# Performance work log

Measured on AMD Instinct MI355X. Metric: run time of the kernel, lower is better.

Reference implementation:

```python
import jax, jax.numpy as jnp
import numpy as np

TAU = 2.0      # LIF membrane time constant
VTH = 1.0      # spike threshold
ALPHA = 2.0    # surrogate-gradient sharpness (atan surrogate)
EPS = 1e-5     # BatchNorm eps

@jax.custom_vjp
def spike(u):
    return (u > 0.0).astype(u.dtype)

def _spike_fwd(u):
    return spike(u), u

def _spike_bwd(u, g):
    sg = ALPHA / (2.0 * (1.0 + (jnp.pi / 2.0 * ALPHA * u) ** 2))
    return (g * sg,)

spike.defvjp(_spike_fwd, _spike_bwd)

def lif_time(x):
    # x: [B,T,C,H,W] -> spikes [B,T,C,H,W]; hard-reset LIF, v0 = 0
    xT = jnp.moveaxis(x, 1, 0)  # [T,B,C,H,W]
    def step(v, xt):
        v = v + (xt - v) / TAU
        s = spike(v - VTH)
        return v * (1.0 - s), s
    _, sT = jax.lax.scan(step, jnp.zeros_like(xT[0]), xT)
    return jnp.moveaxis(sT, 0, 1)

def conv2d(x, w, stride, pad):
    return jax.lax.conv_general_dilated(
        x, w, (stride, stride), [(pad, pad), (pad, pad)],
        dimension_numbers=('NCHW', 'OIHW', 'NCHW'))

def bn(x, gamma, beta, mean, var):
    # inference-style BatchNorm2d with running stats; x: [N,C,H,W]
    inv = gamma * jax.lax.rsqrt(var + EPS)
    return x * inv[None, :, None, None] + (beta - mean * inv)[None, :, None, None]

def setup_inputs() -> dict:
    key = jax.random.key(0)
    ks = jax.random.split(key, 16)
    B, T, Cin, Cout, H, W = 16, 8, 128, 256, 56, 56
    d = {}
    d['x_spike'] = (jax.random.uniform(ks[0], (B, T, Cin, H, W)) < 0.2).astype(jnp.float32)
    d['conv1_w'] = jax.random.normal(ks[1], (Cout, Cin, 3, 3), dtype=jnp.float32) * 0.05
    d['conv2_w'] = jax.random.normal(ks[2], (Cout, Cout, 3, 3), dtype=jnp.float32) * 0.05
    d['ds_w'] = jax.random.normal(ks[3], (Cout, Cin, 1, 1), dtype=jnp.float32) * 0.05
    for i, p in enumerate(['n1', 'n2', 'nd']):
        d[p + '_gamma'] = 1.0 + 0.1 * jax.random.normal(ks[4 + i], (Cout,), dtype=jnp.float32)
        d[p + '_beta'] = 0.1 * jax.random.normal(ks[7 + i], (Cout,), dtype=jnp.float32)
        d[p + '_mean'] = 0.01 * jax.random.normal(ks[10 + i], (Cout,), dtype=jnp.float32)
        d[p + '_var'] = jax.random.uniform(ks[13 + i], (Cout,), minval=0.5, maxval=1.5)
    return d

def reference(x_spike, conv1_w, conv2_w, ds_w,
              n1_gamma, n1_beta, n1_mean, n1_var,
              n2_gamma, n2_beta, n2_mean, n2_var,
              nd_gamma, nd_beta, nd_mean, nd_var):
    B, T, Cin, H, W = x_spike.shape
    x_flat = x_spike.reshape(B * T, Cin, H, W)
    # downsample shortcut (1x1 conv stride 2 + BN)
    identity = bn(conv2d(x_flat, ds_w, 2, 0), nd_gamma, nd_beta, nd_mean, nd_var)
    # NOTE: original module runs lif_shortcut on identity but DISCARDS the result
    # (pure state side-effect); it does not affect the output, so it is omitted.
    out = bn(conv2d(x_flat, conv1_w, 2, 1), n1_gamma, n1_beta, n1_mean, n1_var)
    Cout, Ho, Wo = out.shape[1], out.shape[2], out.shape[3]
    out = lif_time(out.reshape(B, T, Cout, Ho, Wo))
    out = bn(conv2d(out.reshape(B * T, Cout, Ho, Wo), conv2_w, 1, 1),
             n2_gamma, n2_beta, n2_mean, n2_var) + identity
    return lif_time(out.reshape(B, T, Cout, Ho, Wo))
```

## Files before the change

### kernel.cpp

```cpp
#include <hip/hip_runtime.h>
#include <hip/hip_bf16.h>

#define CIN  128
#define CO   256
#define HIN  56
#define WIN  56
#define OH   28
#define OWW  28
#define P    784
#define HWIN 3136
#define PERT 200704

typedef __attribute__((ext_vector_type(8))) short bf16x8v;
typedef __attribute__((ext_vector_type(4))) float f32x4;

__device__ __forceinline__ f32x4 mfma16(bf16x8v a, bf16x8v b, f32x4 c) {
    return __builtin_amdgcn_mfma_f32_16x16x32_bf16(a, b, c, 0, 0, 0);
}

__device__ __forceinline__ void gld_lds16(const void* g, void* l) {
    __builtin_amdgcn_global_load_lds(
        (const __attribute__((address_space(1))) void*)g,
        (__attribute__((address_space(3))) void*)l, 16, 0, 0);
}

__global__ __launch_bounds__(256) void k_prep_bias(
    const float* __restrict__ g1, const float* __restrict__ b1,
    const float* __restrict__ m1, const float* __restrict__ v1,
    const float* __restrict__ g2, const float* __restrict__ b2,
    const float* __restrict__ m2, const float* __restrict__ v2,
    const float* __restrict__ gd, const float* __restrict__ bd,
    const float* __restrict__ md, const float* __restrict__ vd,
    float* __restrict__ inv1o, float* __restrict__ bias1o,
    float* __restrict__ inv2o, float* __restrict__ invdo,
    float* __restrict__ bias2o)
{
    int co = threadIdx.x;
    float inv1 = g1[co] / sqrtf(v1[co] + 1e-5f);
    float inv2 = g2[co] / sqrtf(v2[co] + 1e-5f);
    float invd = gd[co] / sqrtf(vd[co] + 1e-5f);
    inv1o[co]  = inv1;
    bias1o[co] = fmaf(-m1[co], inv1, b1[co]);
    inv2o[co]  = inv2;
    invdo[co]  = invd;
    bias2o[co] = fmaf(-m2[co], inv2, b2[co]) + fmaf(-md[co], invd, bd[co]);
}

__global__ __launch_bounds__(256) void k_prep_w2p(
    const float* __restrict__ w2, const float* __restrict__ inv2,
    unsigned short* __restrict__ hi, unsigned short* __restrict__ lo)
{
    int i = blockIdx.x * 256 + threadIdx.x;
    if (i >= 73728) return;
    int tap = i >> 13;
    int r   = i & 8191;
    int ch  = r >> 10;
    int r2  = r & 1023;
    int cf  = r2 >> 6;
    int lane = r2 & 63;
    int co  = cf * 16 + (lane & 15);
    int cib = ch * 32 + (lane >> 4) * 8;
#pragma unroll
    for (int j = 0; j < 8; j++) {
        float w = w2[((size_t)co * CO + cib + j) * 9 + tap] * inv2[co];
        __hip_bfloat16 h = __float2bfloat16(w);
        __hip_bfloat16 l = __float2bfloat16(w - __bfloat162float(h));
        hi[(size_t)i * 8 + j] = *(unsigned short*)&h;
        lo[(size_t)i * 8 + j] = *(unsigned short*)&l;
    }
}

__global__ __launch_bounds__(256) void k_prep_w1p(
    const float* __restrict__ w1, const float* __restrict__ inv1,
    unsigned short* __restrict__ hi, unsigned short* __restrict__ mid,
    unsigned short* __restrict__ lo)
{
    int i = blockIdx.x * 256 + threadIdx.x;
    if (i >= 36864) return;
    int tap = i >> 12;
    int r   = i & 4095;
    int ch  = r >> 10;
    int r2  = r & 1023;
    int cf  = r2 >> 6;
    int lane = r2 & 63;
    int co  = cf * 16 + (lane & 15);
    int cib = ch * 32 + (lane >> 4) * 8;
#pragma unroll
    for (int j = 0; j < 8; j++) {
        float w = w1[((size_t)co * CIN + cib + j) * 9 + tap] * inv1[co];
        __hip_bfloat16 h = __float2bfloat16(w);
        float r1 = w - __bfloat162float(h);
        __hip_bfloat16 m = __float2bfloat16(r1);
        float r2f = r1 - __bfloat162float(m);
        __hip_bfloat16 l = __float2bfloat16(r2f);
        hi[(size_t)i * 8 + j]  = *(unsigned short*)&h;
        mid[(size_t)i * 8 + j] = *(unsigned short*)&m;
        lo[(size_t)i * 8 + j]  = *(unsigned short*)&l;
    }
}

__global__ __launch_bounds__(256) void k_prep_wdp(
    const float* __restrict__ wd, const float* __restrict__ invd,
    unsigned short* __restrict__ hi, unsigned short* __restrict__ lo)
{
    int i = blockIdx.x * 256 + threadIdx.x;
    if (i >= 4096) return;
    int ch  = i >> 10;
    int r2  = i & 1023;
    int cf  = r2 >> 6;
    int lane = r2 & 63;
    int co  = cf * 16 + (lane & 15);
    int cib = ch * 32 + (lane >> 4) * 8;
#pragma unroll
    for (int j = 0; j < 8; j++) {
        float w = wd[(size_t)co * CIN + cib + j] * invd[co];
        __hip_bfloat16 h = __float2bfloat16(w);
        __hip_bfloat16 l = __float2bfloat16(w - __bfloat162float(h));
        hi[(size_t)i * 8 + j] = *(unsigned short*)&h;
        lo[(size_t)i * 8 + j] = *(unsigned short*)&l;
    }
}

__global__ __launch_bounds__(256) void k_pack1(
    const float* __restrict__ x, unsigned int* __restrict__ xt_p)
{
    int i = blockIdx.x * 256 + threadIdx.x;
    int pos = i % HWIN;
    int nw  = i / HWIN;
    int w   = nw & 3;
    int n   = nw >> 2;
    const float* xp = x + ((size_t)n * CIN + w * 32) * HWIN + pos;
    unsigned int word = 0;
#pragma unroll
    for (int ci = 0; ci < 32; ci++)
        if (xp[(size_t)ci * HWIN] != 0.f) word |= (1u << ci);
    xt_p[((size_t)n * HWIN + pos) * 4 + w] = word;
}

__global__ __launch_bounds__(256) void k_conv1_mfma(
    const unsigned int* __restrict__ xt_p,
    const unsigned short* __restrict__ w1hip,
    const unsigned short* __restrict__ w1midp,
    const unsigned short* __restrict__ w1lop,
    const float* __restrict__ bias1,
    float* __restrict__ out)
{
    __shared__ unsigned int XW[4 * 522];

    const int n    = blockIdx.x / 7;
    const int rt   = blockIdx.x - n * 7;
    const int r0   = rt * 4;
    const int tid  = threadIdx.x;
    const int wave = tid >> 6;
    const int lane = tid & 63;
    const int l15  = lane & 15;
    const int quad = lane >> 4;
    const int cf0  = blockIdx.y * 8 + wave * 2;

    const unsigned int* xp_n = xt_p + (size_t)n * HWIN * 4;
    for (int i = tid; i < 513; i += 256) {
        int row = i / 57, c = i - row * 57;
        int irow = 2 * r0 - 1 + row;
        int iw   = c - 1;
        uint4 val = {0u, 0u, 0u, 0u};
        if (irow >= 0 && iw >= 0)
            val = *(const uint4*)(xp_n + (size_t)(irow * WIN + iw) * 4);
        int base = row * 58 + c;
        XW[0 * 522 + base] = val.x;
        XW[1 * 522 + base] = val.y;
        XW[2 * 522 + base] = val.z;
        XW[3 * 522 + base] = val.w;
    }
    __syncthreads();

    int rr[7], cc[7];
#pragma unroll
    for (int f = 0; f < 7; f++) {
        int pos = f * 16 + l15;
        rr[f] = pos / 28;
        cc[f] = pos - rr[f] * 28;
    }

    f32x4 acc[2][7];
#pragma unroll
    for (int g = 0; g < 2; g++)
#pragma unroll
        for (int f = 0; f < 7; f++) acc[g][f] = (f32x4){0.f, 0.f, 0.f, 0.f};

    bf16x8v ch0, cm0, cl0, ch1, cm1, cl1;
    bf16x8v nh0, nm0, nl0, nh1, nm1, nl1;
    {
        size_t b0 = ((size_t)0 * 16 + cf0) * 512 + lane * 8;
        ch0 = *(const bf16x8v*)(w1hip + b0);  cm0 = *(const bf16x8v*)(w1midp + b0);
        cl0 = *(const bf16x8v*)(w1lop + b0);
        ch1 = *(const bf16x8v*)(w1hip + b0 + 512); cm1 = *(const bf16x8v*)(w1midp + b0 + 512);
        cl1 = *(const bf16x8v*)(w1lop + b0 + 512);
        nh0 = ch0; nm0 = cm0; nl0 = cl0; nh1 = ch1; nm1 = cm1; nl1 = cl1;
    }

    for (int c = 0; c < 4; c++) {
        for (int tap = 0; tap < 9; tap++) {
            int rd = c * 9 + tap;
            if (rd < 35) {
                int rn = rd + 1, cn = rn / 9, tn = rn - cn * 9;
                size_t b0 = ((size_t)(tn * 4 + cn) * 16 + cf0) * 512 + lane * 8;
                nh0 = *(const bf16x8v*)(w1hip + b0);  nm0 = *(const bf16x8v*)(w1midp + b0);
                nl0 = *(const bf16x8v*)(w1lop + b0);
                nh1 = *(const bf16x8v*)(w1hip + b0 + 512); nm1 = *(const bf16x8v*)(w1midp + b0 + 512);
                nl1 = *(const bf16x8v*)(w1lop + b0 + 512);
            }
            const int kh = tap / 3, kw = tap - kh * 3;
#pragma unroll
            for (int f = 0; f < 7; f++) {
                unsigned int word = XW[c * 522 + (2 * rr[f] + kh) * 58 + 2 * cc[f] + kw];
                unsigned int byt  = (word >> (quad * 8)) & 0xffu;
                uint4 u;
                u.x = ((byt & 1u)   ? 0x3F80u : 0u) | ((byt & 2u)   ? 0x3F800000u : 0u);
                u.y = ((byt & 4u)   ? 0x3F80u : 0u) | ((byt & 8u)   ? 0x3F800000u : 0u);
                u.z = ((byt & 16u)  ? 0x3F80u : 0u) | ((byt & 32u)  ? 0x3F800000u : 0u);
                u.w = ((byt & 64u)  ? 0x3F80u : 0u) | ((byt & 128u) ? 0x3F800000u : 0u);
                union { uint4 q; bf16x8v v; } cv;
                cv.q = u;
                acc[0][f] = mfma16(ch0, cv.v, acc[0][f]);
                acc[0][f] = mfma16(cm0, cv.v, acc[0][f]);
                acc[0][f] = mfma16(cl0, cv.v, acc[0][f]);
                acc[1][f] = mfma16(ch1, cv.v, acc[1][f]);
                acc[1][f] = mfma16(cm1, cv.v, acc[1][f]);
                acc[1][f] = mfma16(cl1, cv.v, acc[1][f]);
            }
            ch0 = nh0; cm0 = nm0; cl0 = nl0; ch1 = nh1; cm1 = nm1; cl1 = nl1;
        }
    }

#pragma unroll
    for (int g = 0; g < 2; g++)
#pragma unroll
        for (int f = 0; f < 7; f++) {
            int pg = rt * 112 + f * 16 + l15;
#pragma unroll
            for (int reg = 0; reg < 4; reg++) {
                int co = cf0 * 16 + g * 16 + quad * 4 + reg;
                out[((size_t)n * CO + co) * P + pg] = acc[g][f][reg] + bias1[co];
            }
        }
}

__global__ __launch_bounds__(256) void k_lif1t(
    const float* __restrict__ pre, unsigned short* __restrict__ st)
{
    __shared__ unsigned short T[16 * 68];
    const int b   = blockIdx.x;
    const int co0 = blockIdx.y * 64;
    const int p0  = blockIdx.z * 16;
    const int tid  = threadIdx.x;
    const int pcol = tid & 15;
    const int g    = tid >> 4;
    const int pos = p0 + g;
    const int oh  = pos / 28, ow = pos - oh * 28;
    const int f8  = ((((oh + 1) * 30 + ow + 1) >> 1) & 3);
    const int o      = (pcol & 7) >> 1;
    const int no     = o ^ f8;
    const int within = (pcol & 1) * 4;
    const int chp    = (co0 >> 5) + (pcol >> 3);
    float v[4] = {0.f, 0.f, 0.f, 0.f};
    for (int t = 0; t < 8; t++) {
        const float* src = pre + (((size_t)(b * 8 + t)) * CO + co0) * P + p0;
        unsigned short s[4];
#pragma unroll
        for (int j = 0; j < 4; j++) {
            int co = g + 16 * j;
            float xv = src[(size_t)co * P + pcol];
            v[j] = v[j] + (xv - v[j]) * 0.5f;
            bool sp = v[j] > 1.0f;
            s[j] = sp ? 0x3F80 : 0;
            if (sp) v[j] = 0.f;
        }
        __syncthreads();
#pragma unroll
        for (int j = 0; j < 4; j++) T[pcol * 68 + g + 16 * j] = s[j];
        __syncthreads();
        unsigned short* dst = st + (((size_t)(b * 8 + t) * 8 + chp) * P + pos) * 32
                               + no * 8 + within;
        ushort4 ov;
        ov.x = T[g * 68 + pcol * 4 + 0];
        ov.y = T[g * 68 + pcol * 4 + 1];
        ov.z = T[g * 68 + pcol * 4 + 2];
        ov.w = T[g * 68 + pcol * 4 + 3];
        *(ushort4*)dst = ov;
    }
}

__global__ __launch_bounds__(256) void k_conv2_mfma(
    const unsigned short* __restrict__ spike_t,
    const unsigned int* __restrict__ xt_p,
    const unsigned short* __restrict__ w2hip,
    const unsigned short* __restrict__ w2lop,
    const unsigned short* __restrict__ wdhip,
    const unsigned short* __restrict__ wdlop,
    const float* __restrict__ bias2,
    float* __restrict__ out)
{
    __shared__ unsigned short SB[2 * 5760];
    __shared__ unsigned int   XW2[4 * 112];

    const int n    = blockIdx.x / 7;
    const int rt   = blockIdx.x - n * 7;
    const int r0   = rt * 4;
    const int tid  = threadIdx.x;
    const int wave = tid >> 6;
    const int lane = tid & 63;
    const int l15  = lane & 15;
    const int quad = lane >> 4;
    const int cf0  = wave * 4;

    {
        uint4 z = {0u, 0u, 0u, 0u};
        for (int i = tid; i < 1440; i += 256) ((uint4*)SB)[i] = z;
    }
    for (int i = tid; i < 112; i += 256) {
        int r = i / 28, c = i - r * 28;
        uint4 w4 = *(const uint4*)(xt_p + ((size_t)n * HWIN
                    + (2 * (r0 + r)) * WIN + 2 * c) * 4);
        XW2[0 * 112 + i] = w4.x;
        XW2[1 * 112 + i] = w4.y;
        XW2[2 * 112 + i] = w4.z;
        XW2[3 * 112 + i] = w4.w;
    }
    __syncthreads();

    int  g_irow[3], g_lds[3];
    bool g_ok[3];
    int  g_half[3];
#pragma unroll
    for (int k = 0; k < 3; k++) {
        int idx  = wave * 3 + k;
        int row  = idx >> 1, half = idx & 1;
        int irow = r0 - 1 + row;
        g_irow[k] = irow;
        g_half[k] = half;
        g_ok[k]   = ((unsigned)irow < 28u) && (half == 0 || lane < 48);
        g_lds[k]  = row * 1920 + 64 + half * 1024;
    }
    const char* sp_n = (const char*)spike_t + (size_t)n * 8 * P * 64;

#pragma unroll
    for (int k = 0; k < 3; k++)
        if (g_ok[k])
            gld_lds16(sp_n + (size_t)g_irow[k] * 1792 + g_half[k] * 1024 + lane * 16,
                      (char*)SB + g_lds[k]);

    int rr[7], cc[7];
#pragma unroll
    for (int f = 0; f < 7; f++) {
        int pos = f * 16 + l15;
        rr[f] = pos / 28;
        cc[f] = pos - rr[f] * 28;
    }

    f32x4 acc[4][7];
#pragma unroll
    for (int g = 0; g < 4; g++)
#pragma unroll
        for (int f = 0; f < 7; f++) acc[g][f] = (f32x4){0.f, 0.f, 0.f, 0.f};

    for (int c = 0; c < 4; c++) {
        size_t b0 = ((size_t)c * 16 + cf0) * 512 + lane * 8;
        bf16x8v ah[4], al[4];
#pragma unroll
        for (int g = 0; g < 4; g++) {
            ah[g] = *(const bf16x8v*)(wdhip + b0 + g * 512);
            al[g] = *(const bf16x8v*)(wdlop + b0 + g * 512);
        }
#pragma unroll
        for (int f = 0; f < 7; f++) {
            unsigned int word = XW2[c * 112 + rr[f] * 28 + cc[f]];
            unsigned int byt  = (word >> (quad * 8)) & 0xffu;
            uint4 u;
            u.x = ((byt & 1u)   ? 0x3F80u : 0u) | ((byt & 2u)   ? 0x3F800000u : 0u);
            u.y = ((byt & 4u)   ? 0x3F80u : 0u) | ((byt & 8u)   ? 0x3F800000u : 0u);
            u.z = ((byt & 16u)  ? 0x3F80u : 0u) | ((byt & 32u)  ? 0x3F800000u : 0u);
            u.w = ((byt & 64u)  ? 0x3F80u : 0u) | ((byt & 128u) ? 0x3F800000u : 0u);
            union { uint4 q; bf16x8v v; } cv;
            cv.q = u;
#pragma unroll
            for (int g = 0; g < 4; g++) {
                acc[g][f] = mfma16(ah[g], cv.v, acc[g][f]);
                acc[g][f] = mfma16(al[g], cv.v, acc[g][f]);
            }
        }
    }
    __syncthreads();

    bf16x8v cw[8], nx[8];
    {
        size_t b0 = ((size_t)0 * 16 + cf0) * 512 + lane * 8;
#pragma unroll
        for (int g = 0; g < 4; g++) {
            cw[2 * g]     = *(const bf16x8v*)(w2hip + b0 + g * 512);
            cw[2 * g + 1] = *(const bf16x8v*)(w2lop + b0 + g * 512);
            nx[2 * g]     = cw[2 * g];
            nx[2 * g + 1] = cw[2 * g + 1];
        }
    }

    for (int c = 0; c < 8; c++) {
        if (c < 7) {
            const char* base = sp_n + (size_t)(c + 1) * 50176;
            char* dstb = (char*)SB + ((c + 1) & 1) * 11520;
#pragma unroll
            for (int k = 0; k < 3; k++)
                if (g_ok[k])
                    gld_lds16(base + (size_t)g_irow[k] * 1792 + g_half[k] * 1024 + lane * 16,
                              dstb + g_lds[k]);
        }
        const int bufsh = (c & 1) * 5760;
        for (int tap = 0; tap < 9; tap++) {
            int rd = c * 9 + tap;
            if (rd < 71) {
                int rn = rd + 1, cn = rn / 9, tn = rn - cn * 9;
                size_t b0 = ((size_t)(tn * 8 + cn) * 16 + cf0) * 512 + lane * 8;
#pragma unroll
                for (int g = 0; g < 4; g++) {
                    nx[2 * g]     = *(const bf16x8v*)(w2hip + b0 + g * 512);
                    nx[2 * g + 1] = *(const bf16x8v*)(w2lop + b0 + g * 512);
                }
            }
            const int kh = tap / 3, kw = tap - kh * 3;
#pragma unroll
            for (int f = 0; f < 7; f++) {
                int slot = (rr[f] + kh) * 30 + cc[f] + kw;
                int sw   = (slot >> 1) & 3;
                bf16x8v bfr = *(const bf16x8v*)(
                    &SB[bufsh + slot * 32 + ((quad ^ sw) * 8)]);
#pragma unroll
                for (int g = 0; g < 4; g++) {
                    acc[g][f] = mfma16(cw[2 * g], bfr, acc[g][f]);
                    acc[g][f] = mfma16(cw[2 * g + 1], bfr, acc[g][f]);
                }
            }
#pragma unroll
            for (int j = 0; j < 8; j++) cw[j] = nx[j];
        }
        __syncthreads();
    }

#pragma unroll
    for (int g = 0; g < 4; g++)
#pragma unroll
        for (int f = 0; f < 7; f++) {
            int pg = rt * 112 + f * 16 + l15;
#pragma unroll
            for (int reg = 0; reg < 4; reg++) {
                int co = (cf0 + g) * 16 + quad * 4 + reg;
                out[((size_t)n * CO + co) * P + pg] = acc[g][f][reg] + bias2[co];
            }
        }
}

__global__ __launch_bounds__(256) void k_lif4(const float4* __restrict__ in,
                                              float4* __restrict__ out)
{
    const int q = PERT / 4;
    const int i = blockIdx.x * 256 + threadIdx.x;
    const int b = i / q;
    const int r = i - b * q;
    const float4* pi = in  + (size_t)(b * 8) * q + r;
    float4*       po = out + (size_t)(b * 8) * q + r;
    float v0 = 0.f, v1 = 0.f, v2 = 0.f, v3 = 0.f;
#pragma unroll
    for (int t = 0; t < 8; t++) {
        float4 xt = pi[(size_t)t * q];
        float4 s;
        v0 = v0 + (xt.x - v0) * 0.5f; s.x = (v0 > 1.0f) ? 1.f : 0.f; if (v0 > 1.0f) v0 = 0.f;
        v1 = v1 + (xt.y - v1) * 0.5f; s.y = (v1 > 1.0f) ? 1.f : 0.f; if (v1 > 1.0f) v1 = 0.f;
        v2 = v2 + (xt.z - v2) * 0.5f; s.z = (v2 > 1.0f) ? 1.f : 0.f; if (v2 > 1.0f) v2 = 0.f;
        v3 = v3 + (xt.w - v3) * 0.5f; s.w = (v3 > 1.0f) ? 1.f : 0.f; if (v3 > 1.0f) v3 = 0.f;
        po[(size_t)t * q] = s;
    }
}

extern "C" void kernel_launch(void* const* d_in, const int* in_sizes, int n_in,
                              void* d_out, int out_size, void* d_ws, size_t ws_size,
                              hipStream_t stream) {
    const float* x   = (const float*)d_in[0];
    const float* w1  = (const float*)d_in[1];
    const float* w2  = (const float*)d_in[2];
    const float* wd  = (const float*)d_in[3];
    const float* n1g = (const float*)d_in[4];
    const float* n1b = (const float*)d_in[5];
    const float* n1m = (const float*)d_in[6];
    const float* n1v = (const float*)d_in[7];
    const float* n2g = (const float*)d_in[8];
    const float* n2b = (const float*)d_in[9];
    const float* n2m = (const float*)d_in[10];
    const float* n2v = (const float*)d_in[11];
    const float* ndg = (const float*)d_in[12];
    const float* ndb = (const float*)d_in[13];
    const float* ndm = (const float*)d_in[14];
    const float* ndv = (const float*)d_in[15];

    float* out = (float*)d_out;

    char* w = (char*)d_ws;
    unsigned short* spike_t = (unsigned short*)w;
    unsigned short* w2hip   = (unsigned short*)(w + 51380224);
    unsigned short* w2lop   = (unsigned short*)(w + 52559872);
    unsigned short* w1hip   = (unsigned short*)(w + 53739520);
    unsigned short* w1midp  = (unsigned short*)(w + 54329344);
    unsigned short* w1lop   = (unsigned short*)(w + 54919168);
    unsigned short* wdhip   = (unsigned short*)(w + 55508992);
    unsigned short* wdlop   = (unsigned short*)(w + 55574528);
    float*          bias2   = (float*)(w + 55640064);
    float*          bias1   = (float*)(w + 55641088);
    float*          inv1    = (float*)(w + 55642112);
    float*          inv2    = (float*)(w + 55643136);
    float*          invd    = (float*)(w + 55644160);
    unsigned int*   xt_p    = (unsigned int*)(w + 55645184);

    k_prep_bias<<<1, 256, 0, stream>>>(n1g, n1b, n1m, n1v,
                                       n2g, n2b, n2m, n2v,
                                       ndg, ndb, ndm, ndv,
                                       inv1, bias1, inv2, invd, bias2);
    k_prep_w2p<<<288, 256, 0, stream>>>(w2, inv2, w2hip, w2lop);
    k_prep_w1p<<<144, 256, 0, stream>>>(w1, inv1, w1hip, w1midp, w1lop);
    k_prep_wdp<<<16, 256, 0, stream>>>(wd, invd, wdhip, wdlop);

    k_pack1<<<(128 * 4 * HWIN) / 256, 256, 0, stream>>>(x, xt_p);
    k_conv1_mfma<<<dim3(896, 2), 256, 0, stream>>>(
        xt_p, w1hip, w1midp, w1lop, bias1, out);
    k_lif1t<<<dim3(16, 4, 49), 256, 0, stream>>>(out, spike_t);
    k_conv2_mfma<<<dim3(896), 256, 0, stream>>>(
        spike_t, xt_p, w2hip, w2lop, wdhip, wdlop, bias2, out);
    k_lif4<<<(16 * (PERT / 4)) / 256, 256, 0, stream>>>(
        (const float4*)out, (float4*)out);
}
```

Measured before the change: 707.4 us.

## Replace 3-way bf16 split conv1 with exact 24-bit int8 MFMA decomposition

New measurement: 715.0 us. Within noise of the previous version (+1.1%).

```diff
diff --git a/kernel.cpp b/kernel.cpp
--- a/kernel.cpp
+++ b/kernel.cpp
@@ -13,9 +13,14 @@
 
 typedef __attribute__((ext_vector_type(8))) short bf16x8v;
 typedef __attribute__((ext_vector_type(4))) float f32x4;
+typedef __attribute__((ext_vector_type(4))) int   i32x4;
 
 __device__ __forceinline__ f32x4 mfma16(bf16x8v a, bf16x8v b, f32x4 c) {
     return __builtin_amdgcn_mfma_f32_16x16x32_bf16(a, b, c, 0, 0, 0);
+}
+
+__device__ __forceinline__ i32x4 mfma_i8_64(i32x4 a, i32x4 b, i32x4 c) {
+    return __builtin_amdgcn_mfma_i32_16x16x64_i8(a, b, c, 0, 0, 0);
 }
 
 __device__ __forceinline__ void gld_lds16(const void* g, void* l) {
@@ -70,32 +75,55 @@
     }
 }
 
-__global__ __launch_bounds__(256) void k_prep_w1p(
+__global__ __launch_bounds__(256) void k_prep_w1s(
     const float* __restrict__ w1, const float* __restrict__ inv1,
-    unsigned short* __restrict__ hi, unsigned short* __restrict__ mid,
-    unsigned short* __restrict__ lo)
+    float* __restrict__ qscale, float* __restrict__ scale1)
+{
+    int wave = (blockIdx.x * 256 + threadIdx.x) >> 6;
+    int lane = threadIdx.x & 63;
+    int co = wave;
+    float iv = inv1[co];
+    float m = 0.f;
+    for (int k = lane; k < 1152; k += 64)
+        m = fmaxf(m, fabsf(w1[(size_t)co * 1152 + k] * iv));
+#pragma unroll
+    for (int off = 32; off > 0; off >>= 1)
+        m = fmaxf(m, __shfl_xor(m, off));
+    if (lane == 0) {
+        int s = (int)floorf(log2f(8355000.0f / m));
+        if (s > 44) s = 44;
+        qscale[co] = ldexpf(1.0f, s);
+        scale1[co] = ldexpf(1.0f, -s);
+    }
+}
+
+__global__ __launch_bounds__(256) void k_prep_w1i8(
+    const float* __restrict__ w1, const float* __restrict__ inv1,
+    const float* __restrict__ qscale,
+    signed char* __restrict__ pa, signed char* __restrict__ pb,
+    signed char* __restrict__ pc)
 {
     int i = blockIdx.x * 256 + threadIdx.x;
-    if (i >= 36864) return;
-    int tap = i >> 12;
-    int r   = i & 4095;
-    int ch  = r >> 10;
+    if (i >= 18432) return;
+    int tap = i >> 11;
+    int r   = i & 2047;
+    int kg  = r >> 10;
     int r2  = r & 1023;
     int cf  = r2 >> 6;
     int lane = r2 & 63;
     int co  = cf * 16 + (lane & 15);
-    int cib = ch * 32 + (lane >> 4) * 8;
-#pragma unroll
-    for (int j = 0; j < 8; j++) {
-        float w = w1[((size_t)co * CIN + cib + j) * 9 + tap] * inv1[co];
-        __hip_bfloat16 h = __float2bfloat16(w);
-        float r1 = w - __bfloat162float(h);
-        __hip_bfloat16 m = __float2bfloat16(r1);
-        float r2f = r1 - __bfloat162float(m);
-        __hip_bfloat16 l = __float2bfloat16(r2f);
-        hi[(size_t)i * 8 + j]  = *(unsigned short*)&h;
-        mid[(size_t)i * 8 + j] = *(unsigned short*)&m;
-        lo[(size_t)i * 8 + j]  = *(unsigned short*)&l;
+    int ci0 = kg * 64 + (lane >> 4) * 16;
+    float iv = inv1[co], q = qscale[co];
+#pragma unroll
+    for (int j = 0; j < 16; j++) {
+        float w = w1[((size_t)co * CIN + ci0 + j) * 9 + tap] * iv;
+        int W = __float2int_rn(w * q);
+        int d0 = ((W & 0xFF) ^ 0x80) - 0x80;  W = (W - d0) / 256;
+        int d1 = ((W & 0xFF) ^ 0x80) - 0x80;  W = (W - d1) / 256;
+        size_t idx = (size_t)i * 16 + j;
+        pa[idx] = (signed char)W;
+        pb[idx] = (signed char)d1;
+        pc[idx] = (signed char)d0;
     }
 }
 
@@ -139,13 +167,14 @@
 
 __global__ __launch_bounds__(256) void k_conv1_mfma(
     const unsigned int* __restrict__ xt_p,
-    const unsigned short* __restrict__ w1hip,
-    const unsigned short* __restrict__ w1midp,
-    const unsigned short* __restrict__ w1lop,
+    const signed char* __restrict__ pa,
+    const signed char* __restrict__ pb,
+    const signed char* __restrict__ pc,
+    const float* __restrict__ scale1,
     const float* __restrict__ bias1,
     float* __restrict__ out)
 {
-    __shared__ unsigned int XW[4 * 522];
+    __shared__ unsigned int XWP[2][522 * 2];
 
     const int n    = blockIdx.x / 7;
     const int rt   = blockIdx.x - n * 7;
@@ -155,7 +184,7 @@
     const int lane = tid & 63;
     const int l15  = lane & 15;
     const int quad = lane >> 4;
-    const int cf0  = blockIdx.y * 8 + wave * 2;
+    const int cf   = blockIdx.y * 4 + wave;
 
     const unsigned int* xp_n = xt_p + (size_t)n * HWIN * 4;
     for (int i = tid; i < 513; i += 256) {
@@ -166,83 +195,87 @@
         if (irow >= 0 && iw >= 0)
             val = *(const uint4*)(xp_n + (size_t)(irow * WIN + iw) * 4);
         int base = row * 58 + c;
-        XW[0 * 522 + base] = val.x;
-        XW[1 * 522 + base] = val.y;
-        XW[2 * 522 + base] = val.z;
-        XW[3 * 522 + base] = val.w;
+        XWP[0][base * 2 + 0] = val.x;
+        XWP[0][base * 2 + 1] = val.y;
+        XWP[1][base * 2 + 0] = val.z;
+        XWP[1][base * 2 + 1] = val.w;
     }
     __syncthreads();
 
-    int rr[7], cc[7];
+    int ib[7];
 #pragma unroll
     for (int f = 0; f < 7; f++) {
         int pos = f * 16 + l15;
-        rr[f] = pos / 28;
-        cc[f] = pos - rr[f] * 28;
-    }
-
-    f32x4 acc[2][7];
-#pragma unroll
-    for (int g = 0; g < 2; g++)
-#pragma unroll
-        for (int f = 0; f < 7; f++) acc[g][f] = (f32x4){0.f, 0.f, 0.f, 0.f};
-
-    bf16x8v ch0, cm0, cl0, ch1, cm1, cl1;
-    bf16x8v nh0, nm0, nl0, nh1, nm1, nl1;
+        int rr = pos / 28, cc = pos - rr * 28;
+        ib[f] = (2 * rr) * 58 + 2 * cc;
+    }
+
+    const int  qh = quad >> 1;
+    const int  ql = (quad & 1) * 16;
+
+    i32x4 accA[7], accB[7], accC[7];
+#pragma unroll
+    for (int f = 0; f < 7; f++) {
+        accA[f] = (i32x4){0, 0, 0, 0};
+        accB[f] = (i32x4){0, 0, 0, 0};
+        accC[f] = (i32x4){0, 0, 0, 0};
+    }
+
+    i32x4 wa, wb, wc, na, nb, nc;
     {
-        size_t b0 = ((size_t)0 * 16 + cf0) * 512 + lane * 8;
-        ch0 = *(const bf16x8v*)(w1hip + b0);  cm0 = *(const bf16x8v*)(w1midp + b0);
-        cl0 = *(const bf16x8v*)(w1lop + b0);
-        ch1 = *(const bf16x8v*)(w1hip + b0 + 512); cm1 = *(const bf16x8v*)(w1midp + b0 + 512);
-        cl1 = *(const bf16x8v*)(w1lop + b0 + 512);
-        nh0 = ch0; nm0 = cm0; nl0 = cl0; nh1 = ch1; nm1 = cm1; nl1 = cl1;
-    }
-
-    for (int c = 0; c < 4; c++) {
+        size_t b0 = (size_t)cf * 1024 + lane * 16;
+        wa = *(const i32x4*)(pa + b0);
+        wb = *(const i32x4*)(pb + b0);
+        wc = *(const i32x4*)(pc + b0);
+        na = wa; nb = wb; nc = wc;
+    }
+
+    for (int kg = 0; kg < 2; kg++) {
         for (int tap = 0; tap < 9; tap++) {
-            int rd = c * 9 + tap;
-            if (rd < 35) {
-                int rn = rd + 1, cn = rn / 9, tn = rn - cn * 9;
-                size_t b0 = ((size_t)(tn * 4 + cn) * 16 + cf0) * 512 + lane * 8;
-                nh0 = *(const bf16x8v*)(w1hip + b0);  nm0 = *(const bf16x8v*)(w1midp + b0);
-                nl0 = *(const bf16x8v*)(w1lop + b0);
-                nh1 = *(const bf16x8v*)(w1hip + b0 + 512); nm1 = *(const bf16x8v*)(w1midp + b0 + 512);
-                nl1 = *(const bf16x8v*)(w1lop + b0 + 512);
+            int rd = kg * 9 + tap;
+            if (rd < 17) {
+                int rn = rd + 1, kn = rn / 9, tn = rn - kn * 9;
+                size_t b0 = ((size_t)(tn * 2 + kn) * 16 + cf) * 1024 + lane * 16;
+                na = *(const i32x4*)(pa + b0);
+                nb = *(const i32x4*)(pb + b0);
+                nc = *(const i32x4*)(pc + b0);
             }
             const int kh = tap / 3, kw = tap - kh * 3;
+            const int tapoff = kh * 58 + kw;
 #pragma unroll
             for (int f = 0; f < 7; f++) {
-                unsigned int word = XW[c * 522 + (2 * rr[f] + kh) * 58 + 2 * cc[f] + kw];
-                unsigned int byt  = (word >> (quad * 8)) & 0xffu;
+                int base = ib[f] + tapoff;
+                uint2 pr = *(const uint2*)&XWP[kg][base * 2];
+                unsigned int w32  = qh ? pr.y : pr.x;
+                unsigned int bits = (w32 >> ql) & 0xFFFFu;
                 uint4 u;
-                u.x = ((byt & 1u)   ? 0x3F80u : 0u) | ((byt & 2u)   ? 0x3F800000u : 0u);
-                u.y = ((byt & 4u)   ? 0x3F80u : 0u) | ((byt & 8u)   ? 0x3F800000u : 0u);
-                u.z = ((byt & 16u)  ? 0x3F80u : 0u) | ((byt & 32u)  ? 0x3F800000u : 0u);
-                u.w = ((byt & 64u)  ? 0x3F80u : 0u) | ((byt & 128u) ? 0x3F800000u : 0u);
-                union { uint4 q; bf16x8v v; } cv;
+                u.x = ((bits & 15u)         * 0x00204081u) & 0x01010101u;
+                u.y = (((bits >> 4) & 15u)  * 0x00204081u) & 0x01010101u;
+                u.z = (((bits >> 8) & 15u)  * 0x00204081u) & 0x01010101u;
+                u.w = ((bits >> 12)         * 0x00204081u) & 0x01010101u;
+                union { uint4 q; i32x4 v; } cv;
                 cv.q = u;
-                acc[0][f] = mfma16(ch0, cv.v, acc[0][f]);
-                acc[0][f] = mfma16(cm0, cv.v, acc[0][f]);
-                acc[0][f] = mfma16(cl0, cv.v, acc[0][f]);
-                acc[1][f] = mfma16(ch1, cv.v, acc[1][f]);
-                acc[1][f] = mfma16(cm1, cv.v, acc[1][f]);
-                acc[1][f] = mfma16(cl1, cv.v, acc[1][f]);
+                accA[f] = mfma_i8_64(wa, cv.v, accA[f]);
+                accB[f] = mfma_i8_64(wb, cv.v, accB[f]);
+                accC[f] = mfma_i8_64(wc, cv.v, accC[f]);
             }
-            ch0 = nh0; cm0 = nm0; cl0 = nl0; ch1 = nh1; cm1 = nm1; cl1 = nl1;
-        }
-    }
-
-#pragma unroll
-    for (int g = 0; g < 2; g++)
-#pragma unroll
-        for (int f = 0; f < 7; f++) {
-            int pg = rt * 112 + f * 16 + l15;
-#pragma unroll
-            for (int reg = 0; reg < 4; reg++) {
-                int co = cf0 * 16 + g * 16 + quad * 4 + reg;
-                out[((size_t)n * CO + co) * P + pg] = acc[g][f][reg] + bias1[co];
-            }
-        }
+            wa = na; wb = nb; wc = nc;
+        }
+    }
+
+#pragma unroll
+    for (int f = 0; f < 7; f++) {
+        int pg = rt * 112 + f * 16 + l15;
+#pragma unroll
+        for (int reg = 0; reg < 4; reg++) {
+            int co = cf * 16 + quad * 4 + reg;
+            float hi = (float)accA[f][reg];
+            float mi = (float)accB[f][reg];
+            float lo = (float)accC[f][reg];
+            float val = fmaf(hi, 65536.f, fmaf(mi, 256.f, lo));
+            out[((size_t)n * CO + co) * P + pg] = fmaf(val, scale1[co], bias1[co]);
+        }
+    }
 }
 
 __global__ __launch_bounds__(256) void k_lif1t(
@@ -505,9 +538,11 @@
     unsigned short* spike_t = (unsigned short*)w;
     unsigned short* w2hip   = (unsigned short*)(w + 51380224);
     unsigned short* w2lop   = (unsigned short*)(w + 52559872);
-    unsigned short* w1hip   = (unsigned short*)(w + 53739520);
-    unsigned short* w1midp  = (unsigned short*)(w + 54329344);
-    unsigned short* w1lop   = (unsigned short*)(w + 54919168);
+    signed char*    pa      = (signed char*)(w + 53739520);
+    signed char*    pb      = (signed char*)(w + 54034432);
+    signed char*    pc      = (signed char*)(w + 54329344);
+    float*          qscale1 = (float*)(w + 54624256);
+    float*          scale1f = (float*)(w + 54625280);
     unsigned short* wdhip   = (unsigned short*)(w + 55508992);
     unsigned short* wdlop   = (unsigned short*)(w + 55574528);
     float*          bias2   = (float*)(w + 55640064);
@@ -522,12 +557,13 @@
                                        ndg, ndb, ndm, ndv,
                                        inv1, bias1, inv2, invd, bias2);
     k_prep_w2p<<<288, 256, 0, stream>>>(w2, inv2, w2hip, w2lop);
-    k_prep_w1p<<<144, 256, 0, stream>>>(w1, inv1, w1hip, w1midp, w1lop);
+    k_prep_w1s<<<64, 256, 0, stream>>>(w1, inv1, qscale1, scale1f);
+    k_prep_w1i8<<<72, 256, 0, stream>>>(w1, inv1, qscale1, pa, pb, pc);
     k_prep_wdp<<<16, 256, 0, stream>>>(wd, invd, wdhip, wdlop);
 
     k_pack1<<<(128 * 4 * HWIN) / 256, 256, 0, stream>>>(x, xt_p);
-    k_conv1_mfma<<<dim3(896, 2), 256, 0, stream>>>(
-        xt_p, w1hip, w1midp, w1lop, bias1, out);
+    k_conv1_mfma<<<dim3(896, 4), 256, 0, stream>>>(
+        xt_p, pa, pb, pc, scale1f, bias1, out);
     k_lif1t<<<dim3(16, 4, 49), 256, 0, stream>>>(out, spike_t);
     k_conv2_mfma<<<dim3(896), 256, 0, stream>>>(
         spike_t, xt_p, w2hip, w2lop, wdhip, wdlop, bias2, out);
```
